# Performance work log

Measured on AMD Instinct MI355X. Metric: run time of the kernel, lower is better.

Reference implementation:

```python
import jax, jax.numpy as jnp
import numpy as np


def _bilinear(img, gy, gx):
    # img: (H,W); gy,gx: normalized grid coords in [-1,1] (torch grid_sample,
    # bilinear, zeros padding, align_corners=False semantics)
    H, W = img.shape
    y = ((gy + 1.0) * H - 1.0) * 0.5
    x = ((gx + 1.0) * W - 1.0) * 0.5
    y0 = jnp.floor(y); x0 = jnp.floor(x)
    y1 = y0 + 1.0; x1 = x0 + 1.0
    wy1 = y - y0; wx1 = x - x0
    wy0 = 1.0 - wy1; wx0 = 1.0 - wx1

    def gather(yy, xx):
        valid = (yy >= 0) & (yy < H) & (xx >= 0) & (xx < W)
        yc = jnp.clip(yy, 0, H - 1).astype(jnp.int32)
        xc = jnp.clip(xx, 0, W - 1).astype(jnp.int32)
        return jnp.where(valid, img[yc, xc], 0.0)

    return (wy0 * wx0 * gather(y0, x0) + wy0 * wx1 * gather(y0, x1)
            + wy1 * wx0 * gather(y1, x0) + wy1 * wx1 * gather(y1, x1))


_sample = jax.vmap(_bilinear)  # over frames


def setup_inputs() -> dict:
    key = jax.random.key(0)
    ks = jax.random.split(key, 10)
    nframe, batchsize = 16, 1
    H, W = 512, 640
    hp, wp = H - 128, W - 128
    # C/C_back hold pixel coordinates: channel 2i -> y in [0,H], 2i+1 -> x in [0,W]
    scale = jnp.tile(jnp.array([H, W], jnp.float32), nframe)  # (2*nframe,)
    return {
        "y_pred": jax.random.normal(ks[0], (1, nframe - 1, hp, wp), jnp.float32),
        "inp1": jax.random.normal(ks[1], (1, 2, H, W), jnp.float32),
        "inp2": jax.random.normal(ks[2], (1, 2 * nframe, H, W), jnp.float32),
        "inp2_back": jax.random.normal(ks[3], (1, 2 * nframe, H, W), jnp.float32),
        "inp7": 0.1 * jax.random.normal(ks[4], (1, 9 * (nframe - 1)), jnp.float32),
        "inp6": jax.random.normal(ks[5], (1, hp, wp), jnp.float32),
        "inp77": 0.1 * jax.random.normal(ks[6], (1, 9), jnp.float32),
        "nframe": nframe,
        "batchsize": batchsize,
        "C": jax.random.uniform(ks[7], (1, H, W, 2 * nframe), jnp.float32) * scale,
        "C_back": jax.random.uniform(ks[8], (1, H, W, 2 * nframe), jnp.float32) * scale,
        "reg": 1,
        "P1": 1,
        "P2": 1,
    }


def reference(y_pred, inp1, inp2, inp2_back, inp7, inp6, inp77, nframe,
              batchsize, C, C_back, reg, P1, P2):
    # Original torch code is only well-defined for batchsize == 1.
    _, _, H, W = inp1.shape
    hp, wp = y_pred.shape[2], y_pred.shape[3]
    PAD = 64
    dt = y_pred.dtype

    # zero-padded warped-field stacks
    y_pred1 = jnp.zeros((nframe - 1, H, W), dt).at[:, PAD:PAD + hp, PAD:PAD + wp].set(y_pred[0])
    y_pred2 = jnp.zeros((H, W), dt).at[PAD:PAD + hp, PAD:PAD + wp].set(inp6[0])

    # per-frame homography params: inp5 (9, nframe+1), last column zeros
    inp5 = jnp.concatenate([inp77[0][:, None], inp7[0].reshape(9, nframe - 1),
                            jnp.zeros((9, 1), dt)], axis=1)
    a = inp5[0] + 1.0  # (nframe+1,)
    b = inp5[3]
    c = inp5[6]

    # grids: C[..., 2i] -> y, C[..., 2i+1] -> x, normalized to [-1,1]
    Cr = jnp.moveaxis(C[0].reshape(H, W, nframe, 2), 2, 0)       # (nframe,H,W,2)
    Cb = jnp.moveaxis(C_back[0].reshape(H, W, nframe, 2), 2, 0)
    gy = (Cr[..., 0] - H / 2) / (H / 2)
    gx = (Cr[..., 1] - W / 2) / (W / 2)
    gby = (Cb[..., 0] - H / 2) / (H / 2)
    gbx = (Cb[..., 1] - W / 2) / (W / 2)

    warp5 = _sample(y_pred1, gy[:nframe - 1], gx[:nframe - 1])   # (nframe-1,H,W)
    warp6 = _sample(y_pred1, gby[1:nframe], gbx[1:nframe])       # (nframe-1,H,W)

    zero = jnp.zeros((1, H, W), dt)
    warp5f = jnp.concatenate([warp5, zero])        # frame nframe-1 has no forward warp
    warp6f = jnp.concatenate([zero, warp6])        # frame 0 has no backward warp
    prev = jnp.concatenate([y_pred2[None], y_pred1])   # i==0 uses y_pred2, else y_pred1[i-1]
    nxt = jnp.concatenate([y_pred1, zero])             # last frame term is zero

    inp2_r = inp2[0].reshape(nframe, 2, H, W)
    back_r = inp2_back[0].reshape(nframe, 2, H, W)

    ai, bi, ci = a[:nframe, None, None], b[:nframe, None, None], c[:nframe, None, None]
    an, bn, cn = a[1:, None, None], b[1:, None, None], c[1:, None, None]

    diff0 = (ai * inp1[0, 1] + bi * inp1[0, 0] + ci + prev
             - (an * inp2_r[:, 1] + bn * inp2_r[:, 0] + cn + warp5f))
    diff1 = (ai * back_r[:, 1] + bi * back_r[:, 0] + ci + warp6f
             - (an * inp1[0, 1] + bn * inp1[0, 0] + cn + nxt))

    row0 = jnp.mean(diff0.reshape(nframe, -1) ** 2, axis=1)
    row1 = jnp.mean(diff1.reshape(nframe, -1) ** 2, axis=1)
    return jnp.mean(0.5 * (row0 + row1))
```

## Files before the change

### kernel.cpp

```cpp
#include <hip/hip_runtime.h>

#define HH 512
#define WW 640
#define HP 384
#define WP 512
#define PAD 64
#define NF 16
#define HW (HH*WW)
#define PXB 128
#define NPH 8
#define NBLK (HW/PXB)
#define CSTR 34

typedef float vf2 __attribute__((ext_vector_type(2)));

__device__ __forceinline__ float ntload(const float* p) {
    return __builtin_nontemporal_load(p);
}
__device__ __forceinline__ vf2 ntload2(const float* p) {
    return __builtin_nontemporal_load(reinterpret_cast<const vf2*>(p));
}

__device__ __forceinline__ vf2 ld2u(const float* __restrict__ p) {
    vf2 r;
    __builtin_memcpy(&r, p, sizeof(r));
    return r;
}

__device__ __forceinline__ float bsample(const float* __restrict__ yp, int f, float Cy, float Cx) {
    float gy = (Cy - 256.0f) / 256.0f;
    float gx = (Cx - 320.0f) / 320.0f;
    float y = ((gy + 1.0f) * 512.0f - 1.0f) * 0.5f;
    float x = ((gx + 1.0f) * 640.0f - 1.0f) * 0.5f;
    float y0f = floorf(y), x0f = floorf(x);
    float wy1 = y - y0f, wx1 = x - x0f;
    float wy0 = 1.0f - wy1, wx0 = 1.0f - wx1;
    int iy0 = (int)y0f - PAD;
    int ix  = (int)x0f - PAD;
    int ixc = min(max(ix, 0), WP - 2);
    int d   = ix - ixc;

    const float* base = yp + (size_t)f * HP * WP + ixc;
    float r0 = 0.f, r1 = 0.f;
    if ((unsigned)iy0 < HP) {
        vf2 v = ld2u(base + (size_t)iy0 * WP);
        float v0 = (d == 0) ? v.x : ((d == 1)  ? v.y : 0.f);
        float v1 = (d == 0) ? v.y : ((d == -1) ? v.x : 0.f);
        r0 = wx0 * v0 + wx1 * v1;
    }
    if ((unsigned)(iy0 + 1) < HP) {
        vf2 v = ld2u(base + (size_t)(iy0 + 1) * WP);
        float v0 = (d == 0) ? v.x : ((d == 1)  ? v.y : 0.f);
        float v1 = (d == 0) ? v.y : ((d == -1) ? v.x : 0.f);
        r1 = wx0 * v0 + wx1 * v1;
    }
    return wy0 * r0 + wy1 * r1;
}

__device__ __forceinline__ void coef(const float* __restrict__ inp7,
                                     const float* __restrict__ inp77,
                                     int k, float& a, float& b, float& c) {
    if (k == 0)      { a = inp77[0] + 1.0f;  b = inp77[3];     c = inp77[6];     }
    else if (k <= 15){ a = inp7[k-1] + 1.0f; b = inp7[45+k-1]; c = inp7[90+k-1]; }
    else             { a = 1.0f;             b = 0.0f;         c = 0.0f;         }
}

__global__ __launch_bounds__(256, 4) void verloss_main(
    const float* __restrict__ y_pred,
    const float* __restrict__ inp1,
    const float* __restrict__ inp2,
    const float* __restrict__ inp2b,
    const float* __restrict__ inp7,
    const float* __restrict__ inp6,
    const float* __restrict__ inp77,
    const float* __restrict__ C,
    const float* __restrict__ Cb,
    double* __restrict__ partial)
{
    __shared__ float sC [PXB * CSTR];
    __shared__ float sCb[PXB * CSTR];
    __shared__ double sdata[4];

    const int tid  = threadIdx.x;
    const int pxl  = tid >> 1;
    const int kloc = tid & 1;
    const int p    = blockIdx.x * PXB + pxl;

    {
        const float* gC  = C  + (size_t)blockIdx.x * PXB * 32;
        const float* gCb = Cb + (size_t)blockIdx.x * PXB * 32;
        #pragma unroll
        for (int i = 0; i < 8; ++i) {
            int f2 = tid + i * 256;
            int spx = f2 >> 4, sj = f2 & 15;
            vf2 v  = ntload2(gC  + 2 * f2);
            vf2 vb = ntload2(gCb + 2 * f2);
            *reinterpret_cast<vf2*>(&sC [spx * CSTR + 2 * sj]) = v;
            *reinterpret_cast<vf2*>(&sCb[spx * CSTR + 2 * sj]) = vb;
        }
    }

    int y = p / WW, x = p - y * WW;
    int iy = y - PAD, ix = x - PAD;
    bool inpad = ((unsigned)iy < HP) && ((unsigned)ix < WP);
    int padoff = iy * WP + ix;
    float A = inp1[HW + p];
    float B = inp1[p];

    float acc = 0.f;
    __syncthreads();

    for (int g = 0; g < NPH; ++g) {
        int k = 2 * g + kloc;

        float ak, bk, ck, an, bn, cn;
        coef(inp7, inp77, k,     ak, bk, ck);
        coef(inp7, inp77, k + 1, an, bn, cn);

        float prev;
        if (k == 0) prev = inpad ? inp6[padoff] : 0.f;
        else        prev = inpad ? y_pred[(size_t)((k-1)*HP)*WP + padoff] : 0.f;
        float nxt = (k < NF-1 && inpad) ? y_pred[(size_t)(k*HP)*WP + padoff] : 0.f;

        float w5 = 0.f, w6 = 0.f;
        if (k < NF-1) {
            vf2 gg = *reinterpret_cast<const vf2*>(&sC [pxl * CSTR + 2 * k]);
            w5 = bsample(y_pred, k, gg.x, gg.y);
        }
        if (k >= 1) {
            vf2 gg = *reinterpret_cast<const vf2*>(&sCb[pxl * CSTR + 2 * k]);
            w6 = bsample(y_pred, k - 1, gg.x, gg.y);
        }

        float i2hi = ntload(inp2  + (size_t)(2*k+1)*HW + p);
        float i2lo = ntload(inp2  + (size_t)(2*k  )*HW + p);
        float ibhi = ntload(inp2b + (size_t)(2*k+1)*HW + p);
        float iblo = ntload(inp2b + (size_t)(2*k  )*HW + p);

        float d0 = ak*A + bk*B + ck + prev - (an*i2hi + bn*i2lo + cn + w5);
        float d1 = ak*ibhi + bk*iblo + ck + w6 - (an*A + bn*B + cn + nxt);
        acc += d0*d0 + d1*d1;

        if (g < NPH - 1) __syncthreads();
    }

    double v = (double)acc;
    #pragma unroll
    for (int off = 32; off > 0; off >>= 1) v += __shfl_down(v, off, 64);
    int wid = tid >> 6, lane = tid & 63;
    if (lane == 0) sdata[wid] = v;
    __syncthreads();
    if (tid == 0)
        partial[blockIdx.x] = sdata[0] + sdata[1] + sdata[2] + sdata[3];
}

__global__ __launch_bounds__(1024) void verloss_finalize(
    const double* __restrict__ partial, int n, float* __restrict__ out)
{
    double v = 0.0;
    for (int i = threadIdx.x; i < n; i += 1024) v += partial[i];
    #pragma unroll
    for (int off = 32; off > 0; off >>= 1) v += __shfl_down(v, off, 64);
    __shared__ double sdata[16];
    int wid = threadIdx.x >> 6, lane = threadIdx.x & 63;
    if (lane == 0) sdata[wid] = v;
    __syncthreads();
    if (threadIdx.x == 0) {
        double s = 0.0;
        #pragma unroll
        for (int i = 0; i < 16; ++i) s += sdata[i];
        out[0] = (float)(s * (0.5 / ((double)NF * HW)));
    }
}

extern "C" void kernel_launch(void* const* d_in, const int* in_sizes, int n_in,
                              void* d_out, int out_size, void* d_ws, size_t ws_size,
                              hipStream_t stream) {
    const float* y_pred = (const float*)d_in[0];
    const float* inp1   = (const float*)d_in[1];
    const float* inp2   = (const float*)d_in[2];
    const float* inp2b  = (const float*)d_in[3];
    const float* inp7   = (const float*)d_in[4];
    const float* inp6   = (const float*)d_in[5];
    const float* inp77  = (const float*)d_in[6];
    const float* C      = (const float*)d_in[9];
    const float* Cb     = (const float*)d_in[10];
    float* out = (float*)d_out;
    double* partial = (double*)d_ws;

    verloss_main<<<NBLK, 256, 0, stream>>>(y_pred, inp1, inp2, inp2b, inp7,
                                           inp6, inp77, C, Cb, partial);
    verloss_finalize<<<1, 1024, 0, stream>>>(partial, NBLK, out);
}
```

Before: 131.2 us.

## Split forward/backward warp terms across thread pairs to double per-pixel parallelism

Each pixel-frame pair's work is now split across two threads: one computes the forward-warp difference, the other the backward-warp difference, and the results are combined with a lane shuffle. Blocks grow from 256 to 512 threads for the same 128 pixels. The aim is more memory-level parallelism and shorter per-thread dependency chains for the gather-heavy bilinear sampling. The cost is extra threads, a shuffle, some duplicated coefficient and A/B loads, and possible occupancy limits from the larger blocks with launch bounds of 4.

```diff
diff --git a/kernel.cpp b/kernel.cpp
--- a/kernel.cpp
+++ b/kernel.cpp
@@ -7,7 +7,9 @@
 #define PAD 64
 #define NF 16
 #define HW (HH*WW)
+#define FRDW (HP*WP)
 #define PXB 128
+#define NTH 512
 #define NPH 8
 #define NBLK (HW/PXB)
 #define CSTR 34
@@ -40,7 +42,7 @@
     int ixc = min(max(ix, 0), WP - 2);
     int d   = ix - ixc;
 
-    const float* base = yp + (size_t)f * HP * WP + ixc;
+    const float* base = yp + (size_t)f * FRDW + ixc;
     float r0 = 0.f, r1 = 0.f;
     if ((unsigned)iy0 < HP) {
         vf2 v = ld2u(base + (size_t)iy0 * WP);
@@ -65,7 +67,7 @@
     else             { a = 1.0f;             b = 0.0f;         c = 0.0f;         }
 }
 
-__global__ __launch_bounds__(256, 4) void verloss_main(
+__global__ __launch_bounds__(NTH, 4) void verloss_main(
     const float* __restrict__ y_pred,
     const float* __restrict__ inp1,
     const float* __restrict__ inp2,
@@ -79,19 +81,20 @@
 {
     __shared__ float sC [PXB * CSTR];
     __shared__ float sCb[PXB * CSTR];
-    __shared__ double sdata[4];
+    __shared__ double sdata[8];
 
     const int tid  = threadIdx.x;
-    const int pxl  = tid >> 1;
     const int kloc = tid & 1;
+    const int role = (tid >> 1) & 1;
+    const int pxl  = tid >> 2;
     const int p    = blockIdx.x * PXB + pxl;
 
     {
         const float* gC  = C  + (size_t)blockIdx.x * PXB * 32;
         const float* gCb = Cb + (size_t)blockIdx.x * PXB * 32;
         #pragma unroll
-        for (int i = 0; i < 8; ++i) {
-            int f2 = tid + i * 256;
+        for (int i = 0; i < 4; ++i) {
+            int f2 = tid + i * NTH;
             int spx = f2 >> 4, sj = f2 & 15;
             vf2 v  = ntload2(gC  + 2 * f2);
             vf2 vb = ntload2(gCb + 2 * f2);
@@ -117,29 +120,30 @@
         coef(inp7, inp77, k,     ak, bk, ck);
         coef(inp7, inp77, k + 1, an, bn, cn);
 
-        float prev;
-        if (k == 0) prev = inpad ? inp6[padoff] : 0.f;
-        else        prev = inpad ? y_pred[(size_t)((k-1)*HP)*WP + padoff] : 0.f;
-        float nxt = (k < NF-1 && inpad) ? y_pred[(size_t)(k*HP)*WP + padoff] : 0.f;
-
-        float w5 = 0.f, w6 = 0.f;
-        if (k < NF-1) {
-            vf2 gg = *reinterpret_cast<const vf2*>(&sC [pxl * CSTR + 2 * k]);
-            w5 = bsample(y_pred, k, gg.x, gg.y);
+        const float* dbase = role ? y_pred + (size_t)k * FRDW
+                                  : (k == 0 ? inp6 : y_pred + (size_t)(k-1) * FRDW);
+        bool dvalid = inpad && (!role || k < NF - 1);
+        float dterm = dvalid ? dbase[padoff] : 0.f;
+
+        const float* sbase = role ? sCb : sC;
+        vf2 gg = *reinterpret_cast<const vf2*>(sbase + pxl * CSTR + 2 * k);
+        bool wvalid = role ? (k >= 1) : (k < NF - 1);
+        float w = 0.f;
+        if (wvalid) w = bsample(y_pred, k - role, gg.x, gg.y);
+
+        const float* sp = role ? inp2b : inp2;
+        float shi = ntload(sp + (size_t)(2*k+1)*HW + p);
+        float slo = ntload(sp + (size_t)(2*k  )*HW + p);
+
+        float t0 = ak*A + bk*B + ck + dterm - (an*shi + bn*slo + cn + w);
+        float t1 = ak*shi + bk*slo + ck + w - (an*A + bn*B + cn + dterm);
+        float dval = role ? t1 : t0;
+
+        float dsw = __shfl_xor(dval, 2, 64);
+        if (!role) {
+            float d0 = dval, d1 = dsw;
+            acc += d0*d0 + d1*d1;
         }
-        if (k >= 1) {
-            vf2 gg = *reinterpret_cast<const vf2*>(&sCb[pxl * CSTR + 2 * k]);
-            w6 = bsample(y_pred, k - 1, gg.x, gg.y);
-        }
-
-        float i2hi = ntload(inp2  + (size_t)(2*k+1)*HW + p);
-        float i2lo = ntload(inp2  + (size_t)(2*k  )*HW + p);
-        float ibhi = ntload(inp2b + (size_t)(2*k+1)*HW + p);
-        float iblo = ntload(inp2b + (size_t)(2*k  )*HW + p);
-
-        float d0 = ak*A + bk*B + ck + prev - (an*i2hi + bn*i2lo + cn + w5);
-        float d1 = ak*ibhi + bk*iblo + ck + w6 - (an*A + bn*B + cn + nxt);
-        acc += d0*d0 + d1*d1;
 
         if (g < NPH - 1) __syncthreads();
     }
@@ -150,8 +154,12 @@
     int wid = tid >> 6, lane = tid & 63;
     if (lane == 0) sdata[wid] = v;
     __syncthreads();
-    if (tid == 0)
-        partial[blockIdx.x] = sdata[0] + sdata[1] + sdata[2] + sdata[3];
+    if (tid == 0) {
+        double s = 0.0;
+        #pragma unroll
+        for (int i = 0; i < 8; ++i) s += sdata[i];
+        partial[blockIdx.x] = s;
+    }
 }
 
 __global__ __launch_bounds__(1024) void verloss_finalize(
@@ -188,7 +196,7 @@
     float* out = (float*)d_out;
     double* partial = (double*)d_ws;
 
-    verloss_main<<<NBLK, 256, 0, stream>>>(y_pred, inp1, inp2, inp2b, inp7,
+    verloss_main<<<NBLK, NTH, 0, stream>>>(y_pred, inp1, inp2, inp2b, inp7,
                                            inp6, inp77, C, Cb, partial);
     verloss_finalize<<<1, 1024, 0, stream>>>(partial, NBLK, out);
 }
```

New measurement: 153.3 us. 1.17x slower.
